# Performance work log

Measured on AMD Instinct MI355X. Metric: run time of the kernel, lower is better.

The kernel has to match this reference:

```python
import jax, jax.numpy as jnp
import numpy as np

D_MODEL = 64
B, L, N = 16, 96, 325
L2 = 3 * L // 2
OUT_LEN = 48


def _ln(x, g, b, eps=1e-5):
    mu = x.mean(-1, keepdims=True)
    var = ((x - mu) ** 2).mean(-1, keepdims=True)
    return (x - mu) / jnp.sqrt(var + eps) * g + b


def _circ_conv(x, w):
    # x: (B, L, Cin); w: (Cout, Cin, 3) torch layout; circular pad of 1, no bias
    xp = jnp.concatenate([x[:, -1:], x, x[:, :1]], axis=1)
    return jax.lax.conv_general_dilated(
        xp, jnp.transpose(w, (2, 1, 0)), (1,), 'VALID',
        dimension_numbers=('NWC', 'WIO', 'NWC'))


def _attn(qx, kvx, Wq, bq, Wk, bk, Wv, bv, Wo, bo):
    # single head (n_heads=1): FullAttention with scale 1/sqrt(E)
    q = qx @ Wq + bq
    k = kvx @ Wk + bk
    v = kvx @ Wv + bv
    scale = 1.0 / jnp.sqrt(jnp.asarray(q.shape[-1], q.dtype))
    A = jax.nn.softmax(jnp.einsum('ble,bse->bls', q, k) * scale, axis=-1)
    o = jnp.einsum('bls,bsd->bld', A, v)
    return o @ Wo + bo


def setup_inputs() -> dict:
    key = jax.random.key(0)
    ks = jax.random.split(key, 24)
    d = D_MODEL
    dff = 4 * d

    def w(k, shape, s=0.02):
        return jax.random.normal(k, shape, dtype=jnp.float32) * s

    inp = {
        'x_enc': jax.random.normal(ks[0], (B, L, 1, N), dtype=jnp.float32),
        'x_dec': jax.random.normal(ks[1], (B, L2, 1, N), dtype=jnp.float32),
        'adj_matrix': jax.random.normal(ks[2], (N, N), dtype=jnp.float32),
        'out_len': OUT_LEN,
        'enc_conv_w': w(ks[3], (d, 1, 3), 0.5),
        'dec_conv_w': w(ks[4], (d, 1, 3), 0.5),
        'eWq': w(ks[5], (d, d)), 'ebq': jnp.zeros((d,), jnp.float32),
        'eWk': w(ks[6], (d, d)), 'ebk': jnp.zeros((d,), jnp.float32),
        'eWv': w(ks[7], (d, d)), 'ebv': jnp.zeros((d,), jnp.float32),
        'eWo': w(ks[8], (d, d)), 'ebo': jnp.zeros((d,), jnp.float32),
        'ec1_w': w(ks[9], (d, d)), 'ec1_b': jnp.zeros((d,), jnp.float32),
        'ec2_w': w(ks[10], (d, d)), 'ec2_b': jnp.zeros((d,), jnp.float32),
        'en1_g': jnp.ones((d,), jnp.float32), 'en1_b': jnp.zeros((d,), jnp.float32),
        'en2_g': jnp.ones((d,), jnp.float32), 'en2_b': jnp.zeros((d,), jnp.float32),
        'dWq': w(ks[11], (d, d)), 'dbq': jnp.zeros((d,), jnp.float32),
        'dWk': w(ks[12], (d, d)), 'dbk': jnp.zeros((d,), jnp.float32),
        'dWv': w(ks[13], (d, d)), 'dbv': jnp.zeros((d,), jnp.float32),
        'dWo': w(ks[14], (d, d)), 'dbo': jnp.zeros((d,), jnp.float32),
        'dc1_w': w(ks[15], (d, dff)), 'dc1_b': jnp.zeros((dff,), jnp.float32),
        'dc2_w': w(ks[16], (dff, d)), 'dc2_b': jnp.zeros((d,), jnp.float32),
        'dn2_g': jnp.ones((d,), jnp.float32), 'dn2_b': jnp.zeros((d,), jnp.float32),
        'dn3_g': jnp.ones((d,), jnp.float32), 'dn3_b': jnp.zeros((d,), jnp.float32),
        'proj_w': w(ks[17], (d, 1)), 'proj_b': jnp.zeros((1,), jnp.float32),
    }
    return inp


def reference(x_enc, x_dec, adj_matrix, out_len, enc_conv_w, dec_conv_w,
              eWq, ebq, eWk, ebk, eWv, ebv, eWo, ebo,
              ec1_w, ec1_b, ec2_w, ec2_b, en1_g, en1_b, en2_g, en2_b,
              dWq, dbq, dWk, dbk, dWv, dbv, dWo, dbo,
              dc1_w, dc1_b, dc2_w, dc2_b, dn2_g, dn2_b, dn3_g, dn3_b,
              proj_w, proj_b):
    Bsz, Ls, _, Nn = x_enc.shape
    mean = jax.lax.stop_gradient(x_enc.mean(axis=1, keepdims=True))  # (B,1,1,N), detached
    xe = jnp.transpose(x_enc - mean, (0, 3, 1, 2)).reshape(Bsz * Nn, Ls, 1)
    # --- encoder ---
    enc_emb = _circ_conv(xe, enc_conv_w)  # (B*N, L, d)
    a = _attn(enc_emb, enc_emb, eWq, ebq, eWk, ebk, eWv, ebv, eWo, ebo)
    x = _ln(enc_emb + a, en1_g, en1_b)
    y = jax.nn.relu(x @ ec1_w + ec1_b) @ ec2_w + ec2_b  # encoder d_ff == d
    enc_out = _ln(x + y, en2_g, en2_b)
    # --- decoder ---
    L2s = x_dec.shape[1]
    xd = jnp.transpose(x_dec, (0, 3, 1, 2)).reshape(Bsz * Nn, L2s, 1)
    dec_mean = xd[:, :out_len].mean(axis=1, keepdims=True)
    xd = xd.at[:, :out_len].add(-dec_mean)
    dec_emb = _circ_conv(xd, dec_conv_w)
    a = _attn(dec_emb, enc_out, dWq, dbq, dWk, dbk, dWv, dbv, dWo, dbo)
    x = _ln(dec_emb + a, dn2_g, dn2_b)
    y = jax.nn.relu(x @ dc1_w + dc1_b) @ dc2_w + dc2_b  # decoder d_ff == 4d
    dec_out = _ln(x + y, dn3_g, dn3_b)
    out = dec_out @ proj_w + proj_b  # (B*N, L2, 1)
    out = jnp.transpose(out.reshape(Bsz, Nn, L2s, 1), (0, 2, 3, 1)) + mean  # (B, L2, 1, N)
    return out[:, -out_len:]
```

## Files before the change

kernel.cpp:

```cpp
#include <hip/hip_runtime.h>

typedef _Float16 h8 __attribute__((ext_vector_type(8)));
typedef _Float16 h4 __attribute__((ext_vector_type(4)));
typedef _Float16 h2 __attribute__((ext_vector_type(2)));
typedef float    f4 __attribute__((ext_vector_type(4)));

#define MFMA4(a,b,c) __builtin_amdgcn_mfma_f32_16x16x16f16((a),(b),(c),0,0,0)

#define NSEQ  5200
#define NNODE 325
#define LE    96
#define LD    144
#define OUTL  48
#define NTHR  192

#define SVT   104

#define K_OFF    0
#define VT_OFF   6144
#define MISC_OFF 12800
#define LDS_HALVES 13288

#define WSQ(i)   ((i)*4096)
#define WS_DC1   40960
#define WS_DC2   57344
#define WS_BQ    73728
#define WS_TOTAL 73728

struct Params {
  const float* x_enc; const float* x_dec;
  const float* enc_conv_w; const float* dec_conv_w;
  const float* eWq; const float* ebq; const float* eWk; const float* ebk;
  const float* eWv; const float* ebv; const float* eWo; const float* ebo;
  const float* ec1_w; const float* ec1_b; const float* ec2_w; const float* ec2_b;
  const float* en1_g; const float* en1_b; const float* en2_g; const float* en2_b;
  const float* dWq; const float* dbq; const float* dWk; const float* dbk;
  const float* dWv; const float* dbv; const float* dWo; const float* dbo;
  const float* dc1_w; const float* dc1_b; const float* dc2_w; const float* dc2_b;
  const float* dn2_g; const float* dn2_b; const float* dn3_g; const float* dn3_b;
  const float* proj_w; const float* proj_b;
  float* out;
};

__device__ __forceinline__ float wave_sum(float v){
  v += __shfl_xor(v, 32, 64); v += __shfl_xor(v, 16, 64);
  v += __shfl_xor(v,  8, 64); v += __shfl_xor(v,  4, 64);
  v += __shfl_xor(v,  2, 64); v += __shfl_xor(v,  1, 64);
  return v;
}
__device__ __forceinline__ float q_sum(float v){
  v += __shfl_xor(v, 16, 64); v += __shfl_xor(v, 32, 64); return v;
}

__device__ __forceinline__ h4 lo4(h8 v){ return __builtin_shufflevector(v, v, 0,1,2,3); }
__device__ __forceinline__ h4 hi4(h8 v){ return __builtin_shufflevector(v, v, 4,5,6,7); }
__device__ __forceinline__ h8 cat8(h4 a, h4 b){ return __builtin_shufflevector(a, b, 0,1,2,3,4,5,6,7); }

__device__ __forceinline__ h4 pk4(f4 v){
  h2 a = __builtin_bit_cast(h2, __builtin_amdgcn_cvt_pkrtz(v[0], v[1]));
  h2 b = __builtin_bit_cast(h2, __builtin_amdgcn_cvt_pkrtz(v[2], v[3]));
  return __builtin_shufflevector(a, b, 0,1,2,3);
}
__device__ __forceinline__ h4 relu_pk(f4 v){
  f4 r;
  #pragma unroll
  for (int i = 0; i < 4; ++i) r[i] = fmaxf(v[i], 0.f);
  return pk4(r);
}

__device__ __forceinline__ void mm64T2(const _Float16* __restrict__ A,
                                       const h4 ta[4], const h4 tb[4],
                                       f4 oa[4], f4 ob[4], int lane,
                                       const float* __restrict__ bias, int d0){
  #pragma unroll
  for (int nt = 0; nt < 4; ++nt){
    const _Float16* ar = A + (nt*128 + lane)*8;
    h8 w0 = *(const h8*)(ar);
    h8 w1 = *(const h8*)(ar + 512);
    f4 b4 = *(const f4*)(bias + nt*16 + d0);
    f4 ca = b4, cb = b4;
    ca = MFMA4(lo4(w0), ta[0], ca);  cb = MFMA4(lo4(w0), tb[0], cb);
    ca = MFMA4(hi4(w0), ta[1], ca);  cb = MFMA4(hi4(w0), tb[1], cb);
    ca = MFMA4(lo4(w1), ta[2], ca);  cb = MFMA4(lo4(w1), tb[2], cb);
    ca = MFMA4(hi4(w1), ta[3], ca);  cb = MFMA4(hi4(w1), tb[3], cb);
    oa[nt] = ca; ob[nt] = cb;
  }
}
__device__ __forceinline__ void mm64T(const _Float16* __restrict__ A,
                                      const h4 t[4], f4 out[4], int lane,
                                      const float* __restrict__ bias, int d0){
  #pragma unroll
  for (int nt = 0; nt < 4; ++nt){
    const _Float16* ar = A + (nt*128 + lane)*8;
    h8 w0 = *(const h8*)(ar);
    h8 w1 = *(const h8*)(ar + 512);
    f4 c = *(const f4*)(bias + nt*16 + d0);
    c = MFMA4(lo4(w0), t[0], c);
    c = MFMA4(hi4(w0), t[1], c);
    c = MFMA4(lo4(w1), t[2], c);
    c = MFMA4(hi4(w1), t[3], c);
    out[nt] = c;
  }
}

__device__ __forceinline__ void lnT(const f4 vf[4], h4 xt[4],
        const float* __restrict__ g_, const float* __restrict__ b_, int q){
  const int d0 = 4*q;
  float s = 0.f, s2 = 0.f;
  #pragma unroll
  for (int nt = 0; nt < 4; ++nt)
    #pragma unroll
    for (int i = 0; i < 4; ++i){ float v = vf[nt][i]; s += v; s2 = fmaf(v, v, s2); }
  s = q_sum(s); s2 = q_sum(s2);
  float mu = s * (1.f/64.f);
  float rs = rsqrtf(fmaxf(s2 * (1.f/64.f) - mu*mu, 0.f) + 1e-5f);
  #pragma unroll
  for (int nt = 0; nt < 4; ++nt){
    f4 g4 = *(const f4*)(g_ + nt*16 + d0);
    f4 b4 = *(const f4*)(b_ + nt*16 + d0);
    f4 o;
    #pragma unroll
    for (int i = 0; i < 4; ++i){
      float sc = g4[i]*rs;
      o[i] = fmaf(vf[nt][i], sc, fmaf(-mu, sc, b4[i]));
    }
    xt[nt] = pk4(o);
  }
}

__device__ __forceinline__ float scoresT(const h4 qt[4], const _Float16* Kf,
                                         h4 pt[6], int lane){
  f4 s[6];
  #pragma unroll
  for (int st = 0; st < 6; ++st){
    const _Float16* kr = Kf + st*1024 + lane*8;
    h8 w0 = *(const h8*)(kr);
    h8 w1 = *(const h8*)(kr + 512);
    f4 cc = {0.f,0.f,0.f,0.f};
    cc = MFMA4(lo4(w0), qt[0], cc);
    cc = MFMA4(hi4(w0), qt[1], cc);
    cc = MFMA4(lo4(w1), qt[2], cc);
    cc = MFMA4(hi4(w1), qt[3], cc);
    s[st] = cc;
  }
  float sm = 0.f;
  #pragma unroll
  for (int st = 0; st < 6; ++st)
    #pragma unroll
    for (int i = 0; i < 4; ++i){ float e = __expf(s[st][i]); s[st][i] = e; sm += e; }
  sm = q_sum(sm);
  #pragma unroll
  for (int st = 0; st < 6; ++st) pt[st] = pk4(s[st]);
  return 1.f/sm;
}

__device__ __forceinline__ void attnT2(h4 xA[4], h4 xB[4],
        const _Float16* Kf, const _Float16* Vt,
        const _Float16* __restrict__ Wqt, const float* __restrict__ qb,
        const _Float16* __restrict__ Wot, const float* __restrict__ bo,
        const float* __restrict__ g_, const float* __restrict__ b_,
        int lane, int m, int q){
  const int d0 = 4*q;
  f4 cA[4], cB[4];
  mm64T2(Wqt, xA, xB, cA, cB, lane, qb, d0);
  h4 qA[4], qB[4];
  #pragma unroll
  for (int nt = 0; nt < 4; ++nt){ qA[nt] = pk4(cA[nt]); qB[nt] = pk4(cB[nt]); }
  h4 pA[6], pB[6];
  float rA_ = scoresT(qA, Kf, pA, lane);
  float rB_ = scoresT(qB, Kf, pB, lane);
  h8 wo0[4], wo1[4];
  #pragma unroll
  for (int nt = 0; nt < 4; ++nt){
    const _Float16* ar = Wot + (nt*128 + lane)*8;
    wo0[nt] = *(const h8*)(ar);
    wo1[nt] = *(const h8*)(ar + 512);
  }
  h4 otA[4], otB[4];
  #pragma unroll
  for (int nt = 0; nt < 4; ++nt){
    const _Float16* vr = Vt + (nt*16+m)*SVT + 4*q;
    f4 ca0 = {0.f,0.f,0.f,0.f}, cb0 = {0.f,0.f,0.f,0.f};
    f4 ca1 = {0.f,0.f,0.f,0.f}, cb1 = {0.f,0.f,0.f,0.f};
    #pragma unroll
    for (int st = 0; st < 3; ++st){
      h4 v = *(const h4*)(vr + st*16);
      ca0 = MFMA4(v, pA[st], ca0);
      cb0 = MFMA4(v, pB[st], cb0);
    }
    #pragma unroll
    for (int st = 3; st < 6; ++st){
      h4 v = *(const h4*)(vr + st*16);
      ca1 = MFMA4(v, pA[st], ca1);
      cb1 = MFMA4(v, pB[st], cb1);
    }
    otA[nt] = pk4((ca0 + ca1) * rA_);
    otB[nt] = pk4((cb0 + cb1) * rB_);
  }
  f4 vfA[4], vfB[4];
  #pragma unroll
  for (int nt = 0; nt < 4; ++nt){
    f4 b4 = *(const f4*)(bo + nt*16 + d0);
    f4 ca = b4, cb = b4;
    ca = MFMA4(lo4(wo0[nt]), otA[0], ca);  cb = MFMA4(lo4(wo0[nt]), otB[0], cb);
    ca = MFMA4(hi4(wo0[nt]), otA[1], ca);  cb = MFMA4(hi4(wo0[nt]), otB[1], cb);
    ca = MFMA4(lo4(wo1[nt]), otA[2], ca);  cb = MFMA4(lo4(wo1[nt]), otB[2], cb);
    ca = MFMA4(hi4(wo1[nt]), otA[3], ca);  cb = MFMA4(hi4(wo1[nt]), otB[3], cb);
    #pragma unroll
    for (int i = 0; i < 4; ++i){
      vfA[nt][i] = ca[i] + (float)xA[nt][i];
      vfB[nt][i] = cb[i] + (float)xB[nt][i];
    }
  }
  lnT(vfA, xA, g_, b_, q);
  lnT(vfB, xB, g_, b_, q);
}

__device__ __forceinline__ void attnT(h4 xt[4], const _Float16* Kf, const _Float16* Vt,
        const _Float16* __restrict__ Wqt, const float* __restrict__ qb,
        const _Float16* __restrict__ Wot, const float* __restrict__ bo,
        const float* __restrict__ g_, const float* __restrict__ b_,
        int lane, int m, int q){
  const int d0 = 4*q;
  f4 c[4];
  mm64T(Wqt, xt, c, lane, qb, d0);
  h4 qt[4];
  #pragma unroll
  for (int nt = 0; nt < 4; ++nt) qt[nt] = pk4(c[nt]);
  h4 pt[6];
  float r_ = scoresT(qt, Kf, pt, lane);
  h8 wo0[4], wo1[4];
  #pragma unroll
  for (int nt = 0; nt < 4; ++nt){
    const _Float16* ar = Wot + (nt*128 + lane)*8;
    wo0[nt] = *(const h8*)(ar);
    wo1[nt] = *(const h8*)(ar + 512);
  }
  h4 ot[4];
  #pragma unroll
  for (int nt = 0; nt < 4; ++nt){
    const _Float16* vr = Vt + (nt*16+m)*SVT + 4*q;
    f4 c0 = {0.f,0.f,0.f,0.f}, c1 = {0.f,0.f,0.f,0.f};
    #pragma unroll
    for (int st = 0; st < 3; ++st)
      c0 = MFMA4(*(const h4*)(vr + st*16), pt[st], c0);
    #pragma unroll
    for (int st = 3; st < 6; ++st)
      c1 = MFMA4(*(const h4*)(vr + st*16), pt[st], c1);
    ot[nt] = pk4((c0 + c1) * r_);
  }
  f4 vf[4];
  #pragma unroll
  for (int nt = 0; nt < 4; ++nt){
    f4 cc = *(const f4*)(bo + nt*16 + d0);
    cc = MFMA4(lo4(wo0[nt]), ot[0], cc);
    cc = MFMA4(hi4(wo0[nt]), ot[1], cc);
    cc = MFMA4(lo4(wo1[nt]), ot[2], cc);
    cc = MFMA4(hi4(wo1[nt]), ot[3], cc);
    #pragma unroll
    for (int i = 0; i < 4; ++i) vf[nt][i] = cc[i] + (float)xt[nt][i];
  }
  lnT(vf, xt, g_, b_, q);
}

__device__ __forceinline__ void ffnT2(h4 xA[4], h4 xB[4],
        const _Float16* __restrict__ W1t, const float* __restrict__ b1,
        const _Float16* __restrict__ W2t, const float* __restrict__ b2,
        const float* __restrict__ g_, const float* __restrict__ b_,
        int lane, int q){
  const int d0 = 4*q;
  f4 cA[4], cB[4];
  mm64T2(W1t, xA, xB, cA, cB, lane, b1, d0);
  h4 hA[4], hB[4];
  #pragma unroll
  for (int nt = 0; nt < 4; ++nt){ hA[nt] = relu_pk(cA[nt]); hB[nt] = relu_pk(cB[nt]); }
  f4 yA[4], yB[4];
  mm64T2(W2t, hA, hB, yA, yB, lane, b2, d0);
  f4 vfA[4], vfB[4];
  #pragma unroll
  for (int nt = 0; nt < 4; ++nt){
    #pragma unroll
    for (int i = 0; i < 4; ++i){
      vfA[nt][i] = yA[nt][i] + (float)xA[nt][i];
      vfB[nt][i] = yB[nt][i] + (float)xB[nt][i];
    }
  }
  lnT(vfA, xA, g_, b_, q);
  lnT(vfB, xB, g_, b_, q);
}

__device__ __forceinline__ void kvT2(const h4 xA[4], const h4 xB[4], int rA, int rB,
        _Float16* Kf, _Float16* Vt,
        const _Float16* __restrict__ Wkt, const float* __restrict__ bk,
        const _Float16* __restrict__ Wvt, const float* __restrict__ bv,
        int lane, int m, int q){
  const int d0 = 4*q;
  f4 cA[4], cB[4];
  mm64T2(Wkt, xA, xB, cA, cB, lane, bk, d0);
  {
    h4 oA[4], oB[4];
    #pragma unroll
    for (int nt = 0; nt < 4; ++nt){ oA[nt] = pk4(cA[nt]); oB[nt] = pk4(cB[nt]); }
    const int stA = rA >> 4, stB = rB >> 4;
    *(h8*)(Kf + stA*1024       + lane*8) = cat8(oA[0], oA[1]);
    *(h8*)(Kf + stA*1024 + 512 + lane*8) = cat8(oA[2], oA[3]);
    *(h8*)(Kf + stB*1024       + lane*8) = cat8(oB[0], oB[1]);
    *(h8*)(Kf + stB*1024 + 512 + lane*8) = cat8(oB[2], oB[3]);
  }
  mm64T2(Wvt, xA, xB, cA, cB, lane, bv, d0);
  #pragma unroll
  for (int nt = 0; nt < 4; ++nt){
    #pragma unroll
    for (int i = 0; i < 4; ++i){
      Vt[(nt*16 + d0 + i)*SVT + rA + m] = (_Float16)cA[nt][i];
      Vt[(nt*16 + d0 + i)*SVT + rB + m] = (_Float16)cB[nt][i];
    }
  }
}

__device__ __forceinline__ void convT(h4 xt[4], const float* __restrict__ cw,
                                      float xl, float xc, float xr, int q){
  const int d0 = 4*q;
  #pragma unroll
  for (int nt = 0; nt < 4; ++nt){
    const float* w = cw + 3*(nt*16 + d0);
    f4 o;
    #pragma unroll
    for (int i = 0; i < 4; ++i)
      o[i] = fmaf(w[3*i], xl, fmaf(w[3*i+1], xc, w[3*i+2]*xr));
    xt[nt] = pk4(o);
  }
}

__global__ void prep_weights(Params p, _Float16* ws){
  const float* sq[10] = {p.eWq, p.eWk, p.eWv, p.eWo, p.ec1_w, p.ec2_w,
                         p.dWq, p.dWk, p.dWv, p.dWo};
  for (int idx = blockIdx.x*blockDim.x + threadIdx.x; idx < WS_TOTAL;
       idx += gridDim.x*blockDim.x){
    int r  = idx & 4095;
    int h  = r & 7, l = (r>>3) & 63, kt2 = (r>>9) & 1, nt = r>>10;
    int m  = l & 15, q = l >> 4;
    int orow = nt*16 + m;
    int kk   = kt2*32 + (h>>2)*16 + q*4 + (h&3);
    float v;
    if (idx < WS_DC1){
      int mi = idx >> 12;
      float sc = (mi == 0 || mi == 6) ? 0.125f : 1.f;
      v = sq[mi][kk*64 + orow] * sc;
    } else if (idx < WS_DC2){
      int cc = (idx - WS_DC1) >> 12;
      v = p.dc1_w[kk*256 + cc*64 + orow];
    } else {
      int cc = (idx - WS_DC2) >> 12;
      v = p.dc2_w[(cc*64 + kk)*64 + orow];
    }
    ws[idx] = (_Float16)v;
  }
  int t0 = blockIdx.x*blockDim.x + threadIdx.x;
  if (t0 < 128){
    float* qb = (float*)(ws + WS_BQ);
    qb[t0] = (t0 < 64 ? p.ebq[t0] : p.dbq[t0 - 64]) * 0.125f;
  }
}

__global__ void __launch_bounds__(NTHR)
__attribute__((amdgpu_waves_per_eu(3, 4)))
GraphTransformer_90237262889124_kernel(Params p, const _Float16* __restrict__ ws)
{
  __shared__ __align__(16) _Float16 lds[LDS_HALVES];
  _Float16* Kf   = lds + K_OFF;
  _Float16* Vt   = lds + VT_OFF;
  float*    serE = (float*)(lds + MISC_OFF);
  float*    serD = serE + 96;
  float*    stat = serD + 144;

  const int tid = threadIdx.x, lane = tid & 63, wave = tid >> 6;
  const int m = lane & 15, q = lane >> 4;
  const int d0 = 4*q;
  const int b = blockIdx.x / NNODE, n = blockIdx.x % NNODE;

  const _Float16* eWq_t = ws + WSQ(0);
  const _Float16* eWk_t = ws + WSQ(1);
  const _Float16* eWv_t = ws + WSQ(2);
  const _Float16* eWo_t = ws + WSQ(3);
  const _Float16* ec1_t = ws + WSQ(4);
  const _Float16* ec2_t = ws + WSQ(5);
  const _Float16* dWq_t = ws + WSQ(6);
  const _Float16* dWk_t = ws + WSQ(7);
  const _Float16* dWv_t = ws + WSQ(8);
  const _Float16* dWo_t = ws + WSQ(9);
  const _Float16* dc1f  = ws + WS_DC1;
  const _Float16* dc2f  = ws + WS_DC2;
  const float* qbE = (const float*)(ws + WS_BQ);
  const float* qbD = qbE + 64;

  if (tid < LE) serE[tid] = p.x_enc[(b*LE + tid)*NNODE + n];
  if (tid >= 48) serD[tid - 48] = p.x_dec[(b*LD + (tid - 48))*NNODE + n];
  __syncthreads();
  if (wave == 0){
    float v = serE[lane] + (lane < 32 ? serE[64 + lane] : 0.f);
    float s = wave_sum(v);
    if (lane == 0) stat[0] = s * (1.f/96.f);
  }
  if (wave == 1){
    float v = (lane < OUTL) ? serD[lane] : 0.f;
    float s = wave_sum(v);
    if (lane == 0) stat[1] = s * (1.f/48.f);
  }
  __syncthreads();

  const int rA = wave * 16;
  const int rB = (wave + 3) * 16;
  h4 xA[4], xB[4];
  {
    const float mu = stat[0];
    int lA = rA + m;
    int lmA = lA ? lA-1 : LE-1;
    int lpA = (lA == LE-1) ? 0 : lA+1;
    convT(xA, p.enc_conv_w, serE[lmA]-mu, serE[lA]-mu, serE[lpA]-mu, q);
    int lB = rB + m;
    int lmB = lB - 1;
    int lpB = (lB == LE-1) ? 0 : lB+1;
    convT(xB, p.enc_conv_w, serE[lmB]-mu, serE[lB]-mu, serE[lpB]-mu, q);
    kvT2(xA, xB, rA, rB, Kf, Vt, eWk_t, p.ebk, eWv_t, p.ebv, lane, m, q);
  }
  __syncthreads();
  attnT2(xA, xB, Kf, Vt, eWq_t, qbE, eWo_t, p.ebo, p.en1_g, p.en1_b, lane, m, q);
  ffnT2(xA, xB, ec1_t, p.ec1_b, ec2_t, p.ec2_b, p.en2_g, p.en2_b, lane, q);
  __syncthreads();
  h4 xt[4];
  {
    const float mu = stat[1];
    const int gr = 96 + rA + m;
    float xl = serD[gr-1];
    float xc = serD[gr];
    float xr = (gr == LD-1) ? (serD[0] - mu) : serD[gr+1];
    convT(xt, p.dec_conv_w, xl, xc, xr, q);
  }
  kvT2(xA, xB, rA, rB, Kf, Vt, dWk_t, p.dbk, dWv_t, p.dbv, lane, m, q);
  __syncthreads();
  {
    attnT(xt, Kf, Vt, dWq_t, qbD, dWo_t, p.dbo, p.dn2_g, p.dn2_b, lane, m, q);
    f4 acc[4];
    #pragma unroll
    for (int nt = 0; nt < 4; ++nt) acc[nt] = *(const f4*)(p.dc2_b + nt*16 + d0);
    for (int cc2 = 0; cc2 < 4; ++cc2){
      f4 hh[4];
      mm64T(dc1f + cc2*4096, xt, hh, lane, p.dc1_b + cc2*64, d0);
      h4 ht[4];
      #pragma unroll
      for (int nt = 0; nt < 4; ++nt) ht[nt] = relu_pk(hh[nt]);
      #pragma unroll
      for (int nt = 0; nt < 4; ++nt){
        const _Float16* ar = dc2f + cc2*4096 + (nt*128 + lane)*8;
        h8 w0 = *(const h8*)(ar);
        h8 w1 = *(const h8*)(ar + 512);
        acc[nt] = MFMA4(lo4(w0), ht[0], acc[nt]);
        acc[nt] = MFMA4(hi4(w0), ht[1], acc[nt]);
        acc[nt] = MFMA4(lo4(w1), ht[2], acc[nt]);
        acc[nt] = MFMA4(hi4(w1), ht[3], acc[nt]);
      }
    }
    f4 vf[4];
    #pragma unroll
    for (int nt = 0; nt < 4; ++nt){
      #pragma unroll
      for (int i = 0; i < 4; ++i) vf[nt][i] = acc[nt][i] + (float)xt[nt][i];
    }
    float s = 0.f, s2 = 0.f;
    #pragma unroll
    for (int nt = 0; nt < 4; ++nt)
      #pragma unroll
      for (int i = 0; i < 4; ++i){ float v = vf[nt][i]; s += v; s2 = fmaf(v, v, s2); }
    s = q_sum(s); s2 = q_sum(s2);
    float mu = s * (1.f/64.f);
    float rs = rsqrtf(fmaxf(s2 * (1.f/64.f) - mu*mu, 0.f) + 1e-5f);
    float pp = 0.f;
    #pragma unroll
    for (int nt = 0; nt < 4; ++nt){
      f4 g4 = *(const f4*)(p.dn3_g + nt*16 + d0);
      f4 b4 = *(const f4*)(p.dn3_b + nt*16 + d0);
      f4 w4 = *(const f4*)(p.proj_w + nt*16 + d0);
      #pragma unroll
      for (int i = 0; i < 4; ++i)
        pp += ((vf[nt][i]-mu)*rs*g4[i] + b4[i]) * w4[i];
    }
    pp = q_sum(pp);
    if (q == 0)
      p.out[(b*OUTL + rA + m)*NNODE + n] = pp + p.proj_b[0] + stat[0];
  }
}

extern "C" void kernel_launch(void* const* d_in, const int* in_sizes, int n_in,
                              void* d_out, int out_size, void* d_ws, size_t ws_size,
                              hipStream_t stream) {
  Params p;
  p.x_enc = (const float*)d_in[0];  p.x_dec = (const float*)d_in[1];
  p.enc_conv_w = (const float*)d_in[4];  p.dec_conv_w = (const float*)d_in[5];
  p.eWq = (const float*)d_in[6];   p.ebq = (const float*)d_in[7];
  p.eWk = (const float*)d_in[8];   p.ebk = (const float*)d_in[9];
  p.eWv = (const float*)d_in[10];  p.ebv = (const float*)d_in[11];
  p.eWo = (const float*)d_in[12];  p.ebo = (const float*)d_in[13];
  p.ec1_w = (const float*)d_in[14]; p.ec1_b = (const float*)d_in[15];
  p.ec2_w = (const float*)d_in[16]; p.ec2_b = (const float*)d_in[17];
  p.en1_g = (const float*)d_in[18]; p.en1_b = (const float*)d_in[19];
  p.en2_g = (const float*)d_in[20]; p.en2_b = (const float*)d_in[21];
  p.dWq = (const float*)d_in[22];  p.dbq = (const float*)d_in[23];
  p.dWk = (const float*)d_in[24];  p.dbk = (const float*)d_in[25];
  p.dWv = (const float*)d_in[26];  p.dbv = (const float*)d_in[27];
  p.dWo = (const float*)d_in[28];  p.dbo = (const float*)d_in[29];
  p.dc1_w = (const float*)d_in[30]; p.dc1_b = (const float*)d_in[31];
  p.dc2_w = (const float*)d_in[32]; p.dc2_b = (const float*)d_in[33];
  p.dn2_g = (const float*)d_in[34]; p.dn2_b = (const float*)d_in[35];
  p.dn3_g = (const float*)d_in[36]; p.dn3_b = (const float*)d_in[37];
  p.proj_w = (const float*)d_in[38]; p.proj_b = (const float*)d_in[39];
  p.out = (float*)d_out;

  _Float16* ws = (_Float16*)d_ws;
  prep_weights<<<144, 512, 0, stream>>>(p, ws);
  GraphTransformer_90237262889124_kernel<<<NSEQ, NTHR, 0, stream>>>(p, ws);
}
```

Measured before the change: 276.7 us.

## Double block to six waves, one tile per wave, split decoder FFN across waves

The block grows from 3 to 6 waves so each wave handles one 16-row tile instead of two interleaved tiles, which removes the paired A/B code paths. In the decoder, the 3 query tiles run attention on waves 0-2. The 4-chunk FFN is then split so waves 3-5 compute two hidden chunks and pass their partial sums back through LDS, where waves 0-2 combine them. The occupancy hint moves to 8 waves per EU to rely on more resident waves for latency hiding, at the cost of extra barriers, LDS traffic and idle waves during decoder attention.

```diff
diff --git a/kernel.cpp b/kernel.cpp
--- a/kernel.cpp
+++ b/kernel.cpp
@@ -12,7 +12,7 @@
 #define LE    96
 #define LD    144
 #define OUTL  48
-#define NTHR  192
+#define NTHR  384
 
 #define SVT   104
 
@@ -20,6 +20,9 @@
 #define VT_OFF   6144
 #define MISC_OFF 12800
 #define LDS_HALVES 13288
+
+#define X_OFF    0
+#define P_OFF_H  3072
 
 #define WSQ(i)   ((i)*4096)
 #define WS_DC1   40960
@@ -68,24 +71,6 @@
   return pk4(r);
 }
 
-__device__ __forceinline__ void mm64T2(const _Float16* __restrict__ A,
-                                       const h4 ta[4], const h4 tb[4],
-                                       f4 oa[4], f4 ob[4], int lane,
-                                       const float* __restrict__ bias, int d0){
-  #pragma unroll
-  for (int nt = 0; nt < 4; ++nt){
-    const _Float16* ar = A + (nt*128 + lane)*8;
-    h8 w0 = *(const h8*)(ar);
-    h8 w1 = *(const h8*)(ar + 512);
-    f4 b4 = *(const f4*)(bias + nt*16 + d0);
-    f4 ca = b4, cb = b4;
-    ca = MFMA4(lo4(w0), ta[0], ca);  cb = MFMA4(lo4(w0), tb[0], cb);
-    ca = MFMA4(hi4(w0), ta[1], ca);  cb = MFMA4(hi4(w0), tb[1], cb);
-    ca = MFMA4(lo4(w1), ta[2], ca);  cb = MFMA4(lo4(w1), tb[2], cb);
-    ca = MFMA4(hi4(w1), ta[3], ca);  cb = MFMA4(hi4(w1), tb[3], cb);
-    oa[nt] = ca; ob[nt] = cb;
-  }
-}
 __device__ __forceinline__ void mm64T(const _Float16* __restrict__ A,
                                       const h4 t[4], f4 out[4], int lane,
                                       const float* __restrict__ bias, int d0){
@@ -154,68 +139,6 @@
   return 1.f/sm;
 }
 
-__device__ __forceinline__ void attnT2(h4 xA[4], h4 xB[4],
-        const _Float16* Kf, const _Float16* Vt,
-        const _Float16* __restrict__ Wqt, const float* __restrict__ qb,
-        const _Float16* __restrict__ Wot, const float* __restrict__ bo,
-        const float* __restrict__ g_, const float* __restrict__ b_,
-        int lane, int m, int q){
-  const int d0 = 4*q;
-  f4 cA[4], cB[4];
-  mm64T2(Wqt, xA, xB, cA, cB, lane, qb, d0);
-  h4 qA[4], qB[4];
-  #pragma unroll
-  for (int nt = 0; nt < 4; ++nt){ qA[nt] = pk4(cA[nt]); qB[nt] = pk4(cB[nt]); }
-  h4 pA[6], pB[6];
-  float rA_ = scoresT(qA, Kf, pA, lane);
-  float rB_ = scoresT(qB, Kf, pB, lane);
-  h8 wo0[4], wo1[4];
-  #pragma unroll
-  for (int nt = 0; nt < 4; ++nt){
-    const _Float16* ar = Wot + (nt*128 + lane)*8;
-    wo0[nt] = *(const h8*)(ar);
-    wo1[nt] = *(const h8*)(ar + 512);
-  }
-  h4 otA[4], otB[4];
-  #pragma unroll
-  for (int nt = 0; nt < 4; ++nt){
-    const _Float16* vr = Vt + (nt*16+m)*SVT + 4*q;
-    f4 ca0 = {0.f,0.f,0.f,0.f}, cb0 = {0.f,0.f,0.f,0.f};
-    f4 ca1 = {0.f,0.f,0.f,0.f}, cb1 = {0.f,0.f,0.f,0.f};
-    #pragma unroll
-    for (int st = 0; st < 3; ++st){
-      h4 v = *(const h4*)(vr + st*16);
-      ca0 = MFMA4(v, pA[st], ca0);
-      cb0 = MFMA4(v, pB[st], cb0);
-    }
-    #pragma unroll
-    for (int st = 3; st < 6; ++st){
-      h4 v = *(const h4*)(vr + st*16);
-      ca1 = MFMA4(v, pA[st], ca1);
-      cb1 = MFMA4(v, pB[st], cb1);
-    }
-    otA[nt] = pk4((ca0 + ca1) * rA_);
-    otB[nt] = pk4((cb0 + cb1) * rB_);
-  }
-  f4 vfA[4], vfB[4];
-  #pragma unroll
-  for (int nt = 0; nt < 4; ++nt){
-    f4 b4 = *(const f4*)(bo + nt*16 + d0);
-    f4 ca = b4, cb = b4;
-    ca = MFMA4(lo4(wo0[nt]), otA[0], ca);  cb = MFMA4(lo4(wo0[nt]), otB[0], cb);
-    ca = MFMA4(hi4(wo0[nt]), otA[1], ca);  cb = MFMA4(hi4(wo0[nt]), otB[1], cb);
-    ca = MFMA4(lo4(wo1[nt]), otA[2], ca);  cb = MFMA4(lo4(wo1[nt]), otB[2], cb);
-    ca = MFMA4(hi4(wo1[nt]), otA[3], ca);  cb = MFMA4(hi4(wo1[nt]), otB[3], cb);
-    #pragma unroll
-    for (int i = 0; i < 4; ++i){
-      vfA[nt][i] = ca[i] + (float)xA[nt][i];
-      vfB[nt][i] = cb[i] + (float)xB[nt][i];
-    }
-  }
-  lnT(vfA, xA, g_, b_, q);
-  lnT(vfB, xB, g_, b_, q);
-}
-
 __device__ __forceinline__ void attnT(h4 xt[4], const _Float16* Kf, const _Float16* Vt,
         const _Float16* __restrict__ Wqt, const float* __restrict__ qb,
         const _Float16* __restrict__ Wot, const float* __restrict__ bo,
@@ -229,13 +152,6 @@
   for (int nt = 0; nt < 4; ++nt) qt[nt] = pk4(c[nt]);
   h4 pt[6];
   float r_ = scoresT(qt, Kf, pt, lane);
-  h8 wo0[4], wo1[4];
-  #pragma unroll
-  for (int nt = 0; nt < 4; ++nt){
-    const _Float16* ar = Wot + (nt*128 + lane)*8;
-    wo0[nt] = *(const h8*)(ar);
-    wo1[nt] = *(const h8*)(ar + 512);
-  }
   h4 ot[4];
   #pragma unroll
   for (int nt = 0; nt < 4; ++nt){
@@ -252,69 +168,64 @@
   f4 vf[4];
   #pragma unroll
   for (int nt = 0; nt < 4; ++nt){
+    const _Float16* ar = Wot + (nt*128 + lane)*8;
+    h8 w0 = *(const h8*)(ar);
+    h8 w1 = *(const h8*)(ar + 512);
     f4 cc = *(const f4*)(bo + nt*16 + d0);
-    cc = MFMA4(lo4(wo0[nt]), ot[0], cc);
-    cc = MFMA4(hi4(wo0[nt]), ot[1], cc);
-    cc = MFMA4(lo4(wo1[nt]), ot[2], cc);
-    cc = MFMA4(hi4(wo1[nt]), ot[3], cc);
+    cc = MFMA4(lo4(w0), ot[0], cc);
+    cc = MFMA4(hi4(w0), ot[1], cc);
+    cc = MFMA4(lo4(w1), ot[2], cc);
+    cc = MFMA4(hi4(w1), ot[3], cc);
     #pragma unroll
     for (int i = 0; i < 4; ++i) vf[nt][i] = cc[i] + (float)xt[nt][i];
   }
   lnT(vf, xt, g_, b_, q);
 }
 
-__device__ __forceinline__ void ffnT2(h4 xA[4], h4 xB[4],
+__device__ __forceinline__ void ffnT(h4 xt[4],
         const _Float16* __restrict__ W1t, const float* __restrict__ b1,
         const _Float16* __restrict__ W2t, const float* __restrict__ b2,
         const float* __restrict__ g_, const float* __restrict__ b_,
         int lane, int q){
   const int d0 = 4*q;
-  f4 cA[4], cB[4];
-  mm64T2(W1t, xA, xB, cA, cB, lane, b1, d0);
-  h4 hA[4], hB[4];
-  #pragma unroll
-  for (int nt = 0; nt < 4; ++nt){ hA[nt] = relu_pk(cA[nt]); hB[nt] = relu_pk(cB[nt]); }
-  f4 yA[4], yB[4];
-  mm64T2(W2t, hA, hB, yA, yB, lane, b2, d0);
-  f4 vfA[4], vfB[4];
-  #pragma unroll
-  for (int nt = 0; nt < 4; ++nt){
-    #pragma unroll
-    for (int i = 0; i < 4; ++i){
-      vfA[nt][i] = yA[nt][i] + (float)xA[nt][i];
-      vfB[nt][i] = yB[nt][i] + (float)xB[nt][i];
-    }
-  }
-  lnT(vfA, xA, g_, b_, q);
-  lnT(vfB, xB, g_, b_, q);
-}
-
-__device__ __forceinline__ void kvT2(const h4 xA[4], const h4 xB[4], int rA, int rB,
+  f4 c[4];
+  mm64T(W1t, xt, c, lane, b1, d0);
+  h4 ht[4];
+  #pragma unroll
+  for (int nt = 0; nt < 4; ++nt) ht[nt] = relu_pk(c[nt]);
+  f4 y[4];
+  mm64T(W2t, ht, y, lane, b2, d0);
+  f4 vf[4];
+  #pragma unroll
+  for (int nt = 0; nt < 4; ++nt){
+    #pragma unroll
+    for (int i = 0; i < 4; ++i) vf[nt][i] = y[nt][i] + (float)xt[nt][i];
+  }
+  lnT(vf, xt, g_, b_, q);
+}
+
+__device__ __forceinline__ void kvT(const h4 xt[4], int r0,
         _Float16* Kf, _Float16* Vt,
         const _Float16* __restrict__ Wkt, const float* __restrict__ bk,
         const _Float16* __restrict__ Wvt, const float* __restrict__ bv,
         int lane, int m, int q){
   const int d0 = 4*q;
-  f4 cA[4], cB[4];
-  mm64T2(Wkt, xA, xB, cA, cB, lane, bk, d0);
+  f4 c[4];
+  mm64T(Wkt, xt, c, lane, bk, d0);
   {
-    h4 oA[4], oB[4];
-    #pragma unroll
-    for (int nt = 0; nt < 4; ++nt){ oA[nt] = pk4(cA[nt]); oB[nt] = pk4(cB[nt]); }
-    const int stA = rA >> 4, stB = rB >> 4;
-    *(h8*)(Kf + stA*1024       + lane*8) = cat8(oA[0], oA[1]);
-    *(h8*)(Kf + stA*1024 + 512 + lane*8) = cat8(oA[2], oA[3]);
-    *(h8*)(Kf + stB*1024       + lane*8) = cat8(oB[0], oB[1]);
-    *(h8*)(Kf + stB*1024 + 512 + lane*8) = cat8(oB[2], oB[3]);
-  }
-  mm64T2(Wvt, xA, xB, cA, cB, lane, bv, d0);
-  #pragma unroll
-  for (int nt = 0; nt < 4; ++nt){
-    #pragma unroll
-    for (int i = 0; i < 4; ++i){
-      Vt[(nt*16 + d0 + i)*SVT + rA + m] = (_Float16)cA[nt][i];
-      Vt[(nt*16 + d0 + i)*SVT + rB + m] = (_Float16)cB[nt][i];
-    }
+    h4 o[4];
+    #pragma unroll
+    for (int nt = 0; nt < 4; ++nt) o[nt] = pk4(c[nt]);
+    const int st = r0 >> 4;
+    *(h8*)(Kf + st*1024       + lane*8) = cat8(o[0], o[1]);
+    *(h8*)(Kf + st*1024 + 512 + lane*8) = cat8(o[2], o[3]);
+  }
+  mm64T(Wvt, xt, c, lane, bv, d0);
+  #pragma unroll
+  for (int nt = 0; nt < 4; ++nt){
+    #pragma unroll
+    for (int i = 0; i < 4; ++i)
+      Vt[(nt*16 + d0 + i)*SVT + r0 + m] = (_Float16)c[nt][i];
   }
 }
 
@@ -364,7 +275,7 @@
 }
 
 __global__ void __launch_bounds__(NTHR)
-__attribute__((amdgpu_waves_per_eu(3, 4)))
+__attribute__((amdgpu_waves_per_eu(8, 8)))
 GraphTransformer_90237262889124_kernel(Params p, const _Float16* __restrict__ ws)
 {
   __shared__ __align__(16) _Float16 lds[LDS_HALVES];
@@ -395,7 +306,8 @@
   const float* qbD = qbE + 64;
 
   if (tid < LE) serE[tid] = p.x_enc[(b*LE + tid)*NNODE + n];
-  if (tid >= 48) serD[tid - 48] = p.x_dec[(b*LD + (tid - 48))*NNODE + n];
+  if (tid >= 128 && tid < 128 + LD)
+    serD[tid - 128] = p.x_dec[(b*LD + (tid - 128))*NNODE + n];
   __syncthreads();
   if (wave == 0){
     float v = serE[lane] + (lane < 32 ? serE[64 + lane] : 0.f);
@@ -409,63 +321,91 @@
   }
   __syncthreads();
 
-  const int rA = wave * 16;
-  const int rB = (wave + 3) * 16;
-  h4 xA[4], xB[4];
+  const int rT = wave * 16;
+  h4 xt[4];
   {
     const float mu = stat[0];
-    int lA = rA + m;
-    int lmA = lA ? lA-1 : LE-1;
-    int lpA = (lA == LE-1) ? 0 : lA+1;
-    convT(xA, p.enc_conv_w, serE[lmA]-mu, serE[lA]-mu, serE[lpA]-mu, q);
-    int lB = rB + m;
-    int lmB = lB - 1;
-    int lpB = (lB == LE-1) ? 0 : lB+1;
-    convT(xB, p.enc_conv_w, serE[lmB]-mu, serE[lB]-mu, serE[lpB]-mu, q);
-    kvT2(xA, xB, rA, rB, Kf, Vt, eWk_t, p.ebk, eWv_t, p.ebv, lane, m, q);
-  }
-  __syncthreads();
-  attnT2(xA, xB, Kf, Vt, eWq_t, qbE, eWo_t, p.ebo, p.en1_g, p.en1_b, lane, m, q);
-  ffnT2(xA, xB, ec1_t, p.ec1_b, ec2_t, p.ec2_b, p.en2_g, p.en2_b, lane, q);
-  __syncthreads();
-  h4 xt[4];
-  {
+    const int l  = rT + m;
+    const int lm = l ? l - 1 : LE - 1;
+    const int lp = (l == LE-1) ? 0 : l + 1;
+    convT(xt, p.enc_conv_w, serE[lm]-mu, serE[l]-mu, serE[lp]-mu, q);
+    kvT(xt, rT, Kf, Vt, eWk_t, p.ebk, eWv_t, p.ebv, lane, m, q);
+  }
+  __syncthreads();
+  attnT(xt, Kf, Vt, eWq_t, qbE, eWo_t, p.ebo, p.en1_g, p.en1_b, lane, m, q);
+  ffnT(xt, ec1_t, p.ec1_b, ec2_t, p.ec2_b, p.en2_g, p.en2_b, lane, q);
+  __syncthreads();
+  h4 xd[4];
+  if (wave < 3){
     const float mu = stat[1];
-    const int gr = 96 + rA + m;
+    const int gr = 96 + rT + m;
     float xl = serD[gr-1];
     float xc = serD[gr];
     float xr = (gr == LD-1) ? (serD[0] - mu) : serD[gr+1];
-    convT(xt, p.dec_conv_w, xl, xc, xr, q);
-  }
-  kvT2(xA, xB, rA, rB, Kf, Vt, dWk_t, p.dbk, dWv_t, p.dbv, lane, m, q);
-  __syncthreads();
-  {
-    attnT(xt, Kf, Vt, dWq_t, qbD, dWo_t, p.dbo, p.dn2_g, p.dn2_b, lane, m, q);
-    f4 acc[4];
-    #pragma unroll
-    for (int nt = 0; nt < 4; ++nt) acc[nt] = *(const f4*)(p.dc2_b + nt*16 + d0);
-    for (int cc2 = 0; cc2 < 4; ++cc2){
-      f4 hh[4];
-      mm64T(dc1f + cc2*4096, xt, hh, lane, p.dc1_b + cc2*64, d0);
-      h4 ht[4];
+    convT(xd, p.dec_conv_w, xl, xc, xr, q);
+  }
+  kvT(xt, rT, Kf, Vt, dWk_t, p.dbk, dWv_t, p.dbv, lane, m, q);
+  __syncthreads();
+  if (wave < 3)
+    attnT(xd, Kf, Vt, dWq_t, qbD, dWo_t, p.dbo, p.dn2_g, p.dn2_b, lane, m, q);
+  __syncthreads();
+  if (wave < 3){
+    #pragma unroll
+    for (int nt = 0; nt < 4; ++nt)
+      *(h4*)(lds + X_OFF + wave*1024 + nt*256 + lane*4) = xd[nt];
+  }
+  __syncthreads();
+  h4 xf[4];
+  if (wave >= 3){
+    #pragma unroll
+    for (int nt = 0; nt < 4; ++nt)
+      xf[nt] = *(const h4*)(lds + X_OFF + (wave-3)*1024 + nt*256 + lane*4);
+  } else {
+    #pragma unroll
+    for (int nt = 0; nt < 4; ++nt) xf[nt] = xd[nt];
+  }
+  f4 acc[4];
+  #pragma unroll
+  for (int nt = 0; nt < 4; ++nt){
+    if (wave < 3) acc[nt] = *(const f4*)(p.dc2_b + nt*16 + d0);
+    else          acc[nt] = f4{0.f,0.f,0.f,0.f};
+  }
+  const int cB = (wave < 3) ? 0 : 2;
+  for (int cc2 = cB; cc2 < cB + 2; ++cc2){
+    f4 hh[4];
+    mm64T(dc1f + cc2*4096, xf, hh, lane, p.dc1_b + cc2*64, d0);
+    h4 ht[4];
+    #pragma unroll
+    for (int nt = 0; nt < 4; ++nt) ht[nt] = relu_pk(hh[nt]);
+    #pragma unroll
+    for (int nt = 0; nt < 4; ++nt){
+      const _Float16* ar = dc2f + cc2*4096 + (nt*128 + lane)*8;
+      h8 w0 = *(const h8*)(ar);
+      h8 w1 = *(const h8*)(ar + 512);
+      acc[nt] = MFMA4(lo4(w0), ht[0], acc[nt]);
+      acc[nt] = MFMA4(hi4(w0), ht[1], acc[nt]);
+      acc[nt] = MFMA4(lo4(w1), ht[2], acc[nt]);
+      acc[nt] = MFMA4(hi4(w1), ht[3], acc[nt]);
+    }
+  }
+  float* Pex = (float*)(lds + P_OFF_H);
+  if (wave >= 3){
+    float* Pp = Pex + (wave - 3)*1088;
+    #pragma unroll
+    for (int nt = 0; nt < 4; ++nt)
       #pragma unroll
-      for (int nt = 0; nt < 4; ++nt) ht[nt] = relu_pk(hh[nt]);
-      #pragma unroll
-      for (int nt = 0; nt < 4; ++nt){
-        const _Float16* ar = dc2f + cc2*4096 + (nt*128 + lane)*8;
-        h8 w0 = *(const h8*)(ar);
-        h8 w1 = *(const h8*)(ar + 512);
-        acc[nt] = MFMA4(lo4(w0), ht[0], acc[nt]);
-        acc[nt] = MFMA4(hi4(w0), ht[1], acc[nt]);
-        acc[nt] = MFMA4(lo4(w1), ht[2], acc[nt]);
-        acc[nt] = MFMA4(hi4(w1), ht[3], acc[nt]);
-      }
-    }
+      for (int i = 0; i < 4; ++i)
+        Pp[(nt*16 + d0 + i)*17 + m] = acc[nt][i];
+  }
+  __syncthreads();
+  if (wave < 3){
+    const float* Pp = Pex + wave*1088;
     f4 vf[4];
     #pragma unroll
     for (int nt = 0; nt < 4; ++nt){
       #pragma unroll
-      for (int i = 0; i < 4; ++i) vf[nt][i] = acc[nt][i] + (float)xt[nt][i];
+      for (int i = 0; i < 4; ++i)
+        vf[nt][i] = acc[nt][i] + Pp[(nt*16 + d0 + i)*17 + m] + (float)xd[nt][i];
     }
     float s = 0.f, s2 = 0.f;
     #pragma unroll
@@ -487,7 +427,7 @@
     }
     pp = q_sum(pp);
     if (q == 0)
-      p.out[(b*OUTL + rA + m)*NNODE + n] = pp + p.proj_b[0] + stat[0];
+      p.out[(b*OUTL + rT + m)*NNODE + n] = pp + p.proj_b[0] + stat[0];
   }
 }
 
```

New measurement: 372.9 us. +34.8%, slower.
